# Performance work log

Hardware: AMD Instinct MI355X
Metric: run time of the kernel (lower is better)

The kernel has to match this reference:

```python
import jax, jax.numpy as jnp
import numpy as np

N_NODES = 50000
N_EDGES = 800000
IN_FEATS = 256
OUT_FEATS = 64


def setup_inputs() -> dict:
    key = jax.random.key(0)
    k1, k2, k3, k4, k5, k6 = jax.random.split(key, 6)
    h = jax.random.normal(k1, (N_NODES, IN_FEATS), dtype=jnp.float32)
    norm = jax.random.uniform(k2, (N_NODES, 1), dtype=jnp.float32)
    weight = jax.random.normal(k3, (IN_FEATS, OUT_FEATS), dtype=jnp.float32) * (1.0 / np.sqrt(OUT_FEATS))
    bias = jax.random.normal(k4, (OUT_FEATS,), dtype=jnp.float32) * (1.0 / np.sqrt(OUT_FEATS))
    src = jax.random.randint(k5, (N_EDGES,), 0, N_NODES, dtype=jnp.int32)
    dst = jax.random.randint(k6, (N_EDGES,), 0, N_NODES, dtype=jnp.int32)
    return {"h": h, "norm": norm, "weight": weight, "bias": bias, "src": src, "dst": dst}


def reference(h, norm, weight, bias, src, dst):
    # h: [N, in_feats] -> linear transform
    hw = h @ weight                      # [N, out_feats]
    hw = hw * norm                       # pre-aggregation norm scale
    # update_all(copy_u, sum): out[v] = sum_{(u,v) in E} hw[u]
    msgs = hw[src]                       # [E, out_feats] gather
    agg = jax.ops.segment_sum(msgs, dst, num_segments=N_NODES)  # [N, out_feats]
    out = agg * norm                     # post-aggregation norm scale
    out = out + bias
    return jax.nn.relu(out)
```

## Files before the change

### kernel.cpp

```cpp
#include <hip/hip_runtime.h>

#define NN 50000
#define NE 800000
#define KF 256
#define MF 64

#define NBK 782
#define HB 49
#define EPB 16384
#define CAP 1536
#define GEMMB 196
#define EIDX_CAP (NE + 16 * NBK)

typedef __attribute__((ext_vector_type(8))) short short8;
typedef __attribute__((ext_vector_type(4))) float f32x4;

static __device__ __forceinline__ unsigned short f2bf(float x) {
  unsigned int u = __float_as_uint(x);
  u += 0x7FFF + ((u >> 16) & 1);
  return (unsigned short)(u >> 16);
}
static __device__ __forceinline__ float bf2f(unsigned short u) {
  return __uint_as_float(((unsigned int)u) << 16);
}

__global__ __launch_bounds__(1024) void hist_prepack(
    const int* __restrict__ dst, int* __restrict__ histT,
    const float* __restrict__ W, unsigned short* __restrict__ wtab) {
  const int t = threadIdx.x;
  if (blockIdx.x == HB) {
    for (int f = t; f < 2048; f += 1024) {
      const int m = f & 15;
      const int quad = (f >> 4) & 3;
      const int nt = (f >> 6) & 3;
      const int k0i = f >> 8;
      const int n = nt * 16 + m;
      const int kb = k0i * 32 + quad * 8;
      short8 p;
#pragma unroll
      for (int j = 0; j < 8; ++j) p[j] = (short)f2bf(W[(kb + j) * MF + n]);
      *(short8*)(wtab + (size_t)f * 8) = p;
    }
    return;
  }
  __shared__ int hh[NBK];
  for (int i = t; i < NBK; i += 1024) hh[i] = 0;
  __syncthreads();
  const int base = blockIdx.x * EPB;
#pragma unroll
  for (int i = 0; i < EPB / 1024; ++i) {
    const int e = base + i * 1024 + t;
    if (e < NE) atomicAdd(&hh[dst[e] >> 6], 1);
  }
  __syncthreads();
  for (int i = t; i < NBK; i += 1024) histT[i * 64 + blockIdx.x] = hh[i];
}

__global__ __launch_bounds__(1024, 4) void scatter_gemm(
    const int* __restrict__ src, const int* __restrict__ dst,
    const int* __restrict__ histT, int* __restrict__ eidx,
    int* __restrict__ bucketStart, int* __restrict__ bucketCnt,
    const float* __restrict__ h, const unsigned short* __restrict__ wtab,
    const float* __restrict__ norm, unsigned short* __restrict__ hwb) {
  const int t = threadIdx.x;

  if (blockIdx.x >= HB) {
    const int sub = t >> 8;
    const int tt = t & 255;
    const int lane = tt & 63;
    const int wv = tt >> 6;
    const int m = lane & 15;
    const int quad = lane >> 4;
    const int row0 = (blockIdx.x - HB) * 256 + sub * 64;
    const int arow = row0 + wv * 16 + m;
    const int rowc = (arow < NN) ? arow : (NN - 1);
    const float4* ap = (const float4*)(h + (size_t)rowc * KF + quad * 8);

    float4 a[16];
#pragma unroll
    for (int k = 0; k < 8; ++k) {
      a[2 * k] = ap[k * 8];
      a[2 * k + 1] = ap[k * 8 + 1];
    }
    __builtin_amdgcn_sched_barrier(0);

    short8 af[8];
#pragma unroll
    for (int k = 0; k < 8; ++k) {
      const float4 a0 = a[2 * k];
      const float4 a1 = a[2 * k + 1];
      af[k][0] = (short)f2bf(a0.x); af[k][1] = (short)f2bf(a0.y);
      af[k][2] = (short)f2bf(a0.z); af[k][3] = (short)f2bf(a0.w);
      af[k][4] = (short)f2bf(a1.x); af[k][5] = (short)f2bf(a1.y);
      af[k][6] = (short)f2bf(a1.z); af[k][7] = (short)f2bf(a1.w);
    }
    __builtin_amdgcn_sched_barrier(0);

    f32x4 acc[4];
#pragma unroll
    for (int i = 0; i < 4; ++i) acc[i] = (f32x4){0.f, 0.f, 0.f, 0.f};

    const short8* wp = (const short8*)wtab;
#pragma unroll
    for (int k0i = 0; k0i < 8; ++k0i) {
      const short8* wk = wp + k0i * 4 * 64 + lane;
#pragma unroll
      for (int nt = 0; nt < 4; ++nt) {
        const short8 bf = wk[nt * 64];
        acc[nt] = __builtin_amdgcn_mfma_f32_16x16x32_bf16(af[k0i], bf, acc[nt], 0, 0, 0);
      }
    }

    const int gm0 = row0 + wv * 16 + quad * 4;
    float nrm[4];
#pragma unroll
    for (int r = 0; r < 4; ++r) nrm[r] = (gm0 + r < NN) ? norm[gm0 + r] : 0.f;
#pragma unroll
    for (int nt = 0; nt < 4; ++nt) {
#pragma unroll
      for (int r = 0; r < 4; ++r) {
        const int gm = gm0 + r;
        if (gm < NN) hwb[(size_t)gm * MF + nt * 16 + m] = f2bf(acc[nt][r] * nrm[r]);
      }
    }
    return;
  }

  __shared__ int s[1024];
  __shared__ int cur[NBK];
  int tot = 0, mine = 0;
  if (t < NBK) {
    const int* hp = histT + t * 64;
#pragma unroll
    for (int b = 0; b < HB; ++b) {
      const int v = hp[b];
      if (b < (int)blockIdx.x) mine += v;
      tot += v;
    }
  }
  const int pad = (tot + 15) & ~15;
  s[t] = (t < NBK) ? pad : 0;
  __syncthreads();
  for (int off = 1; off < 1024; off <<= 1) {
    const int a = (t >= off) ? s[t - off] : 0;
    __syncthreads();
    s[t] += a;
    __syncthreads();
  }
  if (t < NBK) {
    const int start = s[t] - pad;
    cur[t] = start + mine;
    if (blockIdx.x == 0) {
      bucketStart[t] = start;
      bucketCnt[t] = tot;
    }
  }
  __syncthreads();
  const int base = blockIdx.x * EPB;
#pragma unroll
  for (int i = 0; i < EPB / 1024; ++i) {
    const int e = base + i * 1024 + t;
    if (e < NE) {
      const int d = dst[e];
      const int pos = atomicAdd(&cur[d >> 6], 1);
      eidx[pos] = (src[e] << 6) | (d & 63);
    }
  }
}

__global__ __launch_bounds__(1024) void sort_gather(
    const int* __restrict__ bucketStart, const int* __restrict__ bucketCnt,
    const int* __restrict__ eidx, int* __restrict__ eidx2,
    const unsigned short* __restrict__ hwb, const float* __restrict__ norm,
    const float* __restrict__ bias, float* __restrict__ out) {
  __shared__ int hcnt[64];
  __shared__ int sBeg[64];
  __shared__ int sCur[64];
  __shared__ int sE[CAP];
  const int t = threadIdx.x;
  const int g = blockIdx.x;
  const int beg = __builtin_amdgcn_readfirstlane(bucketStart[g]);
  const int cnt = __builtin_amdgcn_readfirstlane(bucketCnt[g]);
  if (t < 64) hcnt[t] = 0;
  __syncthreads();
  for (int i = t; i < cnt; i += 1024) atomicAdd(&hcnt[eidx[beg + i] & 63], 1);
  __syncthreads();
  if (t < 64) {
    const int v = hcnt[t];
    int incl = v;
#pragma unroll
    for (int off = 1; off < 64; off <<= 1) {
      const int u = __shfl_up(incl, off, 64);
      if (t >= off) incl += u;
    }
    const int excl = incl - v;
    sBeg[t] = excl;
    sCur[t] = excl;
    hcnt[t] = excl + v;
  }
  __syncthreads();
  const bool inLds = (cnt <= CAP);
  for (int i = t; i < cnt; i += 1024) {
    const int val = eidx[beg + i];
    const int p = atomicAdd(&sCur[val & 63], 1);
    if (inLds) sE[p] = val >> 6;
    else eidx2[beg + p] = val >> 6;
  }
  __syncthreads();

  const int lane = t & 63;
  const int wv = t >> 6;
  const float bi = bias[lane];
#pragma unroll
  for (int nl = wv; nl < 64; nl += 16) {
    const int vtx = g * 64 + nl;
    if (vtx >= NN) continue;
    const int s0i = __builtin_amdgcn_readfirstlane(sBeg[nl]);
    const int e0i = __builtin_amdgcn_readfirstlane(hcnt[nl]);
    float acc = 0.f;
    int i = s0i;
    if (inLds) {
      for (; i + 8 <= e0i; i += 8) {
        const int s0 = sE[i], s1 = sE[i + 1], s2 = sE[i + 2], s3 = sE[i + 3];
        const int s4 = sE[i + 4], s5 = sE[i + 5], s6 = sE[i + 6], s7 = sE[i + 7];
        const unsigned short x0 = hwb[(size_t)s0 * MF + lane];
        const unsigned short x1 = hwb[(size_t)s1 * MF + lane];
        const unsigned short x2 = hwb[(size_t)s2 * MF + lane];
        const unsigned short x3 = hwb[(size_t)s3 * MF + lane];
        const unsigned short x4 = hwb[(size_t)s4 * MF + lane];
        const unsigned short x5 = hwb[(size_t)s5 * MF + lane];
        const unsigned short x6 = hwb[(size_t)s6 * MF + lane];
        const unsigned short x7 = hwb[(size_t)s7 * MF + lane];
        acc += bf2f(x0); acc += bf2f(x1); acc += bf2f(x2); acc += bf2f(x3);
        acc += bf2f(x4); acc += bf2f(x5); acc += bf2f(x6); acc += bf2f(x7);
      }
      for (; i < e0i; ++i) acc += bf2f(hwb[(size_t)sE[i] * MF + lane]);
    } else {
      for (; i + 8 <= e0i; i += 8) {
        const int s0 = eidx2[beg + i], s1 = eidx2[beg + i + 1];
        const int s2 = eidx2[beg + i + 2], s3 = eidx2[beg + i + 3];
        const int s4 = eidx2[beg + i + 4], s5 = eidx2[beg + i + 5];
        const int s6 = eidx2[beg + i + 6], s7 = eidx2[beg + i + 7];
        acc += bf2f(hwb[(size_t)s0 * MF + lane]);
        acc += bf2f(hwb[(size_t)s1 * MF + lane]);
        acc += bf2f(hwb[(size_t)s2 * MF + lane]);
        acc += bf2f(hwb[(size_t)s3 * MF + lane]);
        acc += bf2f(hwb[(size_t)s4 * MF + lane]);
        acc += bf2f(hwb[(size_t)s5 * MF + lane]);
        acc += bf2f(hwb[(size_t)s6 * MF + lane]);
        acc += bf2f(hwb[(size_t)s7 * MF + lane]);
      }
      for (; i < e0i; ++i) acc += bf2f(hwb[(size_t)eidx2[beg + i] * MF + lane]);
    }
    const float o = acc * norm[vtx] + bi;
    out[(size_t)vtx * MF + lane] = fmaxf(o, 0.f);
  }
}

extern "C" void kernel_launch(void* const* d_in, const int* in_sizes, int n_in,
                              void* d_out, int out_size, void* d_ws, size_t ws_size,
                              hipStream_t stream) {
  const float* h = (const float*)d_in[0];
  const float* norm = (const float*)d_in[1];
  const float* W = (const float*)d_in[2];
  const float* bias = (const float*)d_in[3];
  const int* src = (const int*)d_in[4];
  const int* dst = (const int*)d_in[5];
  float* out = (float*)d_out;

  unsigned short* hwb = (unsigned short*)d_ws;
  unsigned short* wtab = hwb + (size_t)NN * MF;
  int* histT = (int*)(wtab + 16384);
  int* bucketStart = histT + NBK * 64;
  int* bucketCnt = bucketStart + ((NBK + 15) & ~15);
  int* eidx = bucketCnt + ((NBK + 15) & ~15);
  int* eidx2 = eidx + ((EIDX_CAP + 15) & ~15);
  const size_t need =
      ((size_t)NN * MF / 2 + 8192 + NBK * 64 + 2 * ((NBK + 15) & ~15) +
       2 * ((EIDX_CAP + 15) & ~15)) * 4;
  if (ws_size < need) return;

  hist_prepack<<<HB + 1, 1024, 0, stream>>>(dst, histT, W, wtab);
  scatter_gemm<<<HB + GEMMB, 1024, 0, stream>>>(
      src, dst, histT, eidx, bucketStart, bucketCnt, h, wtab, norm, hwb);
  sort_gather<<<NBK, 1024, 0, stream>>>(bucketStart, bucketCnt, eidx, eidx2,
                                        hwb, norm, bias, out);
}
```

Before: 150.4 us.

## Replace histogram-scan bucketing with fixed-capacity atomic buckets and LDS atomic accumulation

Removes the separate histogram/prepack kernel and the global prefix scan. Edges now go into fixed-capacity per-bucket slots reserved with global atomics, and any bucket past capacity spills to an overflow list. The gather kernel no longer sorts edges within a bucket. It accumulates messages directly into a 64x64 LDS tile with float atomics, and the weight table is packed into LDS inside each GEMM block. This cuts one launch and the scan/sort passes, at the cost of a memset, LDS atomic contention, nondeterministic summation order, and a bounded overflow list that can silently drop edges beyond its capacity.

```diff
diff --git a/kernel.cpp b/kernel.cpp
--- a/kernel.cpp
+++ b/kernel.cpp
@@ -10,7 +10,7 @@
 #define EPB 16384
 #define CAP 1536
 #define GEMMB 196
-#define EIDX_CAP (NE + 16 * NBK)
+#define OVF_CAP 4096
 
 typedef __attribute__((ext_vector_type(8))) short short8;
 typedef __attribute__((ext_vector_type(4))) float f32x4;
@@ -24,11 +24,16 @@
   return __uint_as_float(((unsigned int)u) << 16);
 }
 
-__global__ __launch_bounds__(1024) void hist_prepack(
-    const int* __restrict__ dst, int* __restrict__ histT,
-    const float* __restrict__ W, unsigned short* __restrict__ wtab) {
+__global__ __launch_bounds__(1024, 4) void scatter_gemm(
+    const int* __restrict__ src, const int* __restrict__ dst,
+    int* __restrict__ gCur, int* __restrict__ gOvf,
+    unsigned int* __restrict__ ovf, int* __restrict__ eidx,
+    const float* __restrict__ h, const float* __restrict__ W,
+    const float* __restrict__ norm, unsigned short* __restrict__ hwb) {
   const int t = threadIdx.x;
-  if (blockIdx.x == HB) {
+
+  if (blockIdx.x >= HB) {
+    __shared__ unsigned short wt[16384];
     for (int f = t; f < 2048; f += 1024) {
       const int m = f & 15;
       const int quad = (f >> 4) & 3;
@@ -39,32 +44,9 @@
       short8 p;
 #pragma unroll
       for (int j = 0; j < 8; ++j) p[j] = (short)f2bf(W[(kb + j) * MF + n]);
-      *(short8*)(wtab + (size_t)f * 8) = p;
-    }
-    return;
-  }
-  __shared__ int hh[NBK];
-  for (int i = t; i < NBK; i += 1024) hh[i] = 0;
-  __syncthreads();
-  const int base = blockIdx.x * EPB;
-#pragma unroll
-  for (int i = 0; i < EPB / 1024; ++i) {
-    const int e = base + i * 1024 + t;
-    if (e < NE) atomicAdd(&hh[dst[e] >> 6], 1);
-  }
-  __syncthreads();
-  for (int i = t; i < NBK; i += 1024) histT[i * 64 + blockIdx.x] = hh[i];
-}
-
-__global__ __launch_bounds__(1024, 4) void scatter_gemm(
-    const int* __restrict__ src, const int* __restrict__ dst,
-    const int* __restrict__ histT, int* __restrict__ eidx,
-    int* __restrict__ bucketStart, int* __restrict__ bucketCnt,
-    const float* __restrict__ h, const unsigned short* __restrict__ wtab,
-    const float* __restrict__ norm, unsigned short* __restrict__ hwb) {
-  const int t = threadIdx.x;
-
-  if (blockIdx.x >= HB) {
+      *(short8*)(wt + (size_t)f * 8) = p;
+    }
+
     const int sub = t >> 8;
     const int tt = t & 255;
     const int lane = tt & 63;
@@ -95,15 +77,16 @@
       af[k][6] = (short)f2bf(a1.z); af[k][7] = (short)f2bf(a1.w);
     }
     __builtin_amdgcn_sched_barrier(0);
+    __syncthreads();
 
     f32x4 acc[4];
 #pragma unroll
     for (int i = 0; i < 4; ++i) acc[i] = (f32x4){0.f, 0.f, 0.f, 0.f};
 
-    const short8* wp = (const short8*)wtab;
+    const short8* wp = (const short8*)wt;
 #pragma unroll
     for (int k0i = 0; k0i < 8; ++k0i) {
-      const short8* wk = wp + k0i * 4 * 64 + lane;
+      const short8* wk = wp + k0i * 256 + lane;
 #pragma unroll
       for (int nt = 0; nt < 4; ++nt) {
         const short8 bf = wk[nt * 64];
@@ -126,134 +109,106 @@
     return;
   }
 
-  __shared__ int s[1024];
-  __shared__ int cur[NBK];
-  int tot = 0, mine = 0;
-  if (t < NBK) {
-    const int* hp = histT + t * 64;
-#pragma unroll
-    for (int b = 0; b < HB; ++b) {
-      const int v = hp[b];
-      if (b < (int)blockIdx.x) mine += v;
-      tot += v;
-    }
-  }
-  const int pad = (tot + 15) & ~15;
-  s[t] = (t < NBK) ? pad : 0;
-  __syncthreads();
-  for (int off = 1; off < 1024; off <<= 1) {
-    const int a = (t >= off) ? s[t - off] : 0;
-    __syncthreads();
-    s[t] += a;
-    __syncthreads();
-  }
-  if (t < NBK) {
-    const int start = s[t] - pad;
-    cur[t] = start + mine;
-    if (blockIdx.x == 0) {
-      bucketStart[t] = start;
-      bucketCnt[t] = tot;
-    }
-  }
-  __syncthreads();
-  const int base = blockIdx.x * EPB;
+  __shared__ int hh[NBK];
+  __shared__ int bb[NBK];
+  const int base = (int)blockIdx.x * EPB;
+  unsigned int ev[EPB / 1024];
 #pragma unroll
   for (int i = 0; i < EPB / 1024; ++i) {
     const int e = base + i * 1024 + t;
-    if (e < NE) {
-      const int d = dst[e];
-      const int pos = atomicAdd(&cur[d >> 6], 1);
-      eidx[pos] = (src[e] << 6) | (d & 63);
-    }
-  }
-}
-
-__global__ __launch_bounds__(1024) void sort_gather(
-    const int* __restrict__ bucketStart, const int* __restrict__ bucketCnt,
-    const int* __restrict__ eidx, int* __restrict__ eidx2,
+    ev[i] = (e < NE) ? (((unsigned)src[e] << 16) | (unsigned)dst[e])
+                     : 0xFFFFFFFFu;
+  }
+  for (int i = t; i < NBK; i += 1024) hh[i] = 0;
+  __syncthreads();
+#pragma unroll
+  for (int i = 0; i < EPB / 1024; ++i)
+    if (ev[i] != 0xFFFFFFFFu) atomicAdd(&hh[(ev[i] & 0xFFFFu) >> 6], 1);
+  __syncthreads();
+  for (int i = t; i < NBK; i += 1024) {
+    const int c = hh[i];
+    bb[i] = c ? atomicAdd(&gCur[i], c) : 0;
+  }
+  __syncthreads();
+#pragma unroll
+  for (int i = 0; i < EPB / 1024; ++i) {
+    const unsigned v = ev[i];
+    if (v != 0xFFFFFFFFu) {
+      const int d = (int)(v & 0xFFFFu);
+      const int bk = d >> 6;
+      const int p = atomicAdd(&bb[bk], 1);
+      if (p < CAP) {
+        eidx[(size_t)bk * CAP + p] = (int)((v >> 16) << 6) | (d & 63);
+      } else {
+        const int o = atomicAdd(gOvf, 1);
+        if (o < OVF_CAP) ovf[o] = v;
+      }
+    }
+  }
+}
+
+__global__ __launch_bounds__(1024, 4) void gather_acc(
+    const int* __restrict__ gCur, const int* __restrict__ gOvf,
+    const unsigned int* __restrict__ ovf, const int* __restrict__ eidx,
     const unsigned short* __restrict__ hwb, const float* __restrict__ norm,
     const float* __restrict__ bias, float* __restrict__ out) {
-  __shared__ int hcnt[64];
-  __shared__ int sBeg[64];
-  __shared__ int sCur[64];
-  __shared__ int sE[CAP];
+  __shared__ float acc[4096];
   const int t = threadIdx.x;
   const int g = blockIdx.x;
-  const int beg = __builtin_amdgcn_readfirstlane(bucketStart[g]);
-  const int cnt = __builtin_amdgcn_readfirstlane(bucketCnt[g]);
-  if (t < 64) hcnt[t] = 0;
-  __syncthreads();
-  for (int i = t; i < cnt; i += 1024) atomicAdd(&hcnt[eidx[beg + i] & 63], 1);
-  __syncthreads();
-  if (t < 64) {
-    const int v = hcnt[t];
-    int incl = v;
-#pragma unroll
-    for (int off = 1; off < 64; off <<= 1) {
-      const int u = __shfl_up(incl, off, 64);
-      if (t >= off) incl += u;
-    }
-    const int excl = incl - v;
-    sBeg[t] = excl;
-    sCur[t] = excl;
-    hcnt[t] = excl + v;
-  }
-  __syncthreads();
-  const bool inLds = (cnt <= CAP);
-  for (int i = t; i < cnt; i += 1024) {
-    const int val = eidx[beg + i];
-    const int p = atomicAdd(&sCur[val & 63], 1);
-    if (inLds) sE[p] = val >> 6;
-    else eidx2[beg + p] = val >> 6;
-  }
-  __syncthreads();
-
+  ((f32x4*)acc)[t] = (f32x4){0.f, 0.f, 0.f, 0.f};
+  int cnt = gCur[g];
+  cnt = (cnt < CAP) ? cnt : CAP;
+  cnt = __builtin_amdgcn_readfirstlane(cnt);
   const int lane = t & 63;
-  const int wv = t >> 6;
+  const int wv = __builtin_amdgcn_readfirstlane(t >> 6);
+  __syncthreads();
+
+  const int chunk = (cnt + 15) >> 4;
+  const int i0 = wv * chunk;
+  const int iend = ((i0 + chunk) < cnt) ? (i0 + chunk) : cnt;
+  const int* ep = eidx + (size_t)g * CAP;
+  int i = i0;
+  int vv[16];
+  float xx[16];
+  for (; i + 16 <= iend; i += 16) {
+#pragma unroll
+    for (int j = 0; j < 16; ++j) vv[j] = ep[i + j];
+#pragma unroll
+    for (int j = 0; j < 16; ++j)
+      xx[j] = bf2f(hwb[(size_t)(vv[j] >> 6) * MF + lane]);
+    __builtin_amdgcn_sched_barrier(0);
+#pragma unroll
+    for (int j = 0; j < 16; ++j)
+      atomicAdd(&acc[((vv[j] & 63) << 6) + lane], xx[j]);
+  }
+  for (; i < iend; ++i) {
+    const int v = ep[i];
+    const float x = bf2f(hwb[(size_t)(v >> 6) * MF + lane]);
+    atomicAdd(&acc[((v & 63) << 6) + lane], x);
+  }
+
+  const int no = *gOvf;
+  if (no > 0) {
+    const int nn = (no < OVF_CAP) ? no : OVF_CAP;
+    for (int ii = wv; ii < nn; ii += 16) {
+      const unsigned v = ovf[ii];
+      const int d = (int)(v & 0xFFFFu);
+      if ((d >> 6) == g) {
+        const float x = bf2f(hwb[(size_t)(v >> 16) * MF + lane]);
+        atomicAdd(&acc[((d & 63) << 6) + lane], x);
+      }
+    }
+  }
+  __syncthreads();
+
   const float bi = bias[lane];
 #pragma unroll
-  for (int nl = wv; nl < 64; nl += 16) {
-    const int vtx = g * 64 + nl;
-    if (vtx >= NN) continue;
-    const int s0i = __builtin_amdgcn_readfirstlane(sBeg[nl]);
-    const int e0i = __builtin_amdgcn_readfirstlane(hcnt[nl]);
-    float acc = 0.f;
-    int i = s0i;
-    if (inLds) {
-      for (; i + 8 <= e0i; i += 8) {
-        const int s0 = sE[i], s1 = sE[i + 1], s2 = sE[i + 2], s3 = sE[i + 3];
-        const int s4 = sE[i + 4], s5 = sE[i + 5], s6 = sE[i + 6], s7 = sE[i + 7];
-        const unsigned short x0 = hwb[(size_t)s0 * MF + lane];
-        const unsigned short x1 = hwb[(size_t)s1 * MF + lane];
-        const unsigned short x2 = hwb[(size_t)s2 * MF + lane];
-        const unsigned short x3 = hwb[(size_t)s3 * MF + lane];
-        const unsigned short x4 = hwb[(size_t)s4 * MF + lane];
-        const unsigned short x5 = hwb[(size_t)s5 * MF + lane];
-        const unsigned short x6 = hwb[(size_t)s6 * MF + lane];
-        const unsigned short x7 = hwb[(size_t)s7 * MF + lane];
-        acc += bf2f(x0); acc += bf2f(x1); acc += bf2f(x2); acc += bf2f(x3);
-        acc += bf2f(x4); acc += bf2f(x5); acc += bf2f(x6); acc += bf2f(x7);
-      }
-      for (; i < e0i; ++i) acc += bf2f(hwb[(size_t)sE[i] * MF + lane]);
-    } else {
-      for (; i + 8 <= e0i; i += 8) {
-        const int s0 = eidx2[beg + i], s1 = eidx2[beg + i + 1];
-        const int s2 = eidx2[beg + i + 2], s3 = eidx2[beg + i + 3];
-        const int s4 = eidx2[beg + i + 4], s5 = eidx2[beg + i + 5];
-        const int s6 = eidx2[beg + i + 6], s7 = eidx2[beg + i + 7];
-        acc += bf2f(hwb[(size_t)s0 * MF + lane]);
-        acc += bf2f(hwb[(size_t)s1 * MF + lane]);
-        acc += bf2f(hwb[(size_t)s2 * MF + lane]);
-        acc += bf2f(hwb[(size_t)s3 * MF + lane]);
-        acc += bf2f(hwb[(size_t)s4 * MF + lane]);
-        acc += bf2f(hwb[(size_t)s5 * MF + lane]);
-        acc += bf2f(hwb[(size_t)s6 * MF + lane]);
-        acc += bf2f(hwb[(size_t)s7 * MF + lane]);
-      }
-      for (; i < e0i; ++i) acc += bf2f(hwb[(size_t)eidx2[beg + i] * MF + lane]);
-    }
-    const float o = acc * norm[vtx] + bi;
-    out[(size_t)vtx * MF + lane] = fmaxf(o, 0.f);
+  for (int n = wv; n < 64; n += 16) {
+    const int vtx = (g << 6) + n;
+    if (vtx < NN) {
+      const float o = acc[(n << 6) + lane] * norm[vtx] + bi;
+      out[(size_t)vtx * MF + lane] = fmaxf(o, 0.f);
+    }
   }
 }
 
@@ -269,20 +224,17 @@
   float* out = (float*)d_out;
 
   unsigned short* hwb = (unsigned short*)d_ws;
-  unsigned short* wtab = hwb + (size_t)NN * MF;
-  int* histT = (int*)(wtab + 16384);
-  int* bucketStart = histT + NBK * 64;
-  int* bucketCnt = bucketStart + ((NBK + 15) & ~15);
-  int* eidx = bucketCnt + ((NBK + 15) & ~15);
-  int* eidx2 = eidx + ((EIDX_CAP + 15) & ~15);
-  const size_t need =
-      ((size_t)NN * MF / 2 + 8192 + NBK * 64 + 2 * ((NBK + 15) & ~15) +
-       2 * ((EIDX_CAP + 15) & ~15)) * 4;
+  int* gCur = (int*)(hwb + (size_t)NN * MF);
+  int* gOvf = gCur + NBK;
+  unsigned int* ovf = (unsigned int*)(gOvf + 1);
+  int* eidx = (int*)(ovf + OVF_CAP);
+  const size_t need = (size_t)NN * MF * 2 +
+                      ((size_t)NBK + 1 + OVF_CAP + (size_t)NBK * CAP) * 4;
   if (ws_size < need) return;
 
-  hist_prepack<<<HB + 1, 1024, 0, stream>>>(dst, histT, W, wtab);
-  scatter_gemm<<<HB + GEMMB, 1024, 0, stream>>>(
-      src, dst, histT, eidx, bucketStart, bucketCnt, h, wtab, norm, hwb);
-  sort_gather<<<NBK, 1024, 0, stream>>>(bucketStart, bucketCnt, eidx, eidx2,
-                                        hwb, norm, bias, out);
-}
+  hipMemsetAsync(gCur, 0, (NBK + 1) * sizeof(int), stream);
+  scatter_gemm<<<HB + GEMMB, 1024, 0, stream>>>(src, dst, gCur, gOvf, ovf,
+                                                eidx, h, W, norm, hwb);
+  gather_acc<<<NBK, 1024, 0, stream>>>(gCur, gOvf, ovf, eidx, hwb, norm, bias,
+                                       out);
+}
```

Result: slower. 447.1 us (+197.3%).
